# Kernel optimization log

Measured on AMD Instinct MI355X. Metric: run time of the kernel, lower is better.

## Reference

```python
import jax, jax.numpy as jnp
import numpy as np

N, K, IN_DIM, OUT_DIM = 100000, 16, 64, 64
BN_EPS = 1e-5


def setup_inputs() -> dict:
    key = jax.random.key(0)
    ks = jax.random.split(key, 12)
    def lin(k, fan_in, shape):
        bound = 1.0 / np.sqrt(fan_in)
        return jax.random.uniform(k, shape, jnp.float32, -bound, bound)
    return {
        'points': jax.random.normal(ks[0], (N, 3), jnp.float32),
        'neighbors': jax.random.randint(ks[1], (N, K), 0, N + 1, jnp.int32),
        'feats': jax.random.normal(ks[2], (N, IN_DIM), jnp.float32),
        'q_w': lin(ks[3], IN_DIM, (OUT_DIM, IN_DIM)), 'q_b': lin(ks[3], IN_DIM, (OUT_DIM,)),
        'k_w': lin(ks[4], IN_DIM, (OUT_DIM, IN_DIM)), 'k_b': lin(ks[4], IN_DIM, (OUT_DIM,)),
        'v_w': lin(ks[5], IN_DIM, (OUT_DIM, IN_DIM)), 'v_b': lin(ks[5], IN_DIM, (OUT_DIM,)),
        'p_w': lin(ks[6], 3, (OUT_DIM, 3)), 'p_b': lin(ks[6], 3, (OUT_DIM,)),
        'p_gamma': jnp.ones((OUT_DIM,), jnp.float32), 'p_beta': jnp.zeros((OUT_DIM,), jnp.float32),
        'w_w': lin(ks[7], OUT_DIM, (OUT_DIM, OUT_DIM)), 'w_b': lin(ks[7], OUT_DIM, (OUT_DIM,)),
        'w_gamma': jnp.ones((OUT_DIM,), jnp.float32), 'w_beta': jnp.zeros((OUT_DIM,), jnp.float32),
    }


def _bn_relu(x, gamma, beta):
    # BatchNorm1d (training mode, biased var) over all axes except channel (last), then ReLU
    mean = jnp.mean(x, axis=(0, 1), keepdims=True)
    var = jnp.mean(jnp.square(x - mean), axis=(0, 1), keepdims=True)
    y = (x - mean) * jax.lax.rsqrt(var + BN_EPS) * gamma + beta
    return jax.nn.relu(y)


def reference(points, neighbors, feats, q_w, q_b, k_w, k_b, v_w, v_b,
              p_w, p_b, p_gamma, p_beta, w_w, w_b, w_gamma, w_beta):
    q = feats @ q_w.T + q_b                       # [N, D]
    k = feats @ k_w.T + k_b
    v = feats @ v_w.T + v_b
    # shadow-pad with an out-of-range point / zero feats
    points_pad = jnp.concatenate([points, jnp.full((1, 3), 1e6, points.dtype)], 0)
    k_pad = jnp.concatenate([k, jnp.zeros((1, k.shape[1]), k.dtype)], 0)
    v_pad = jnp.concatenate([v, jnp.zeros((1, v.shape[1]), v.dtype)], 0)
    p_g = points_pad[neighbors]                   # [N, K, 3]
    k_g = k_pad[neighbors]                        # [N, K, D]
    v_g = v_pad[neighbors]                        # [N, K, D]
    p_feats = _bn_relu(p_g @ p_w.T + p_b, p_gamma, p_beta)          # [N, K, D]
    w = k_g * q[:, None, :] + p_feats                               # [N, K, D]
    w = _bn_relu(w @ w_w.T + w_b, w_gamma, w_beta)
    w = jax.nn.softmax(w, axis=1)                 # softmax over neighbor axis
    att = jnp.sum((v_g + p_feats) * w, axis=1)    # [N, D]
    return att
```

## Files before the change

### kernel.cpp

```cpp
#include <hip/hip_runtime.h>
#include <math.h>

#define NP 100000
#define KN 16
#define DIM 64
constexpr float BN_EPS_F = 1e-5f;
constexpr double MS = (double)NP * (double)KN;

typedef __attribute__((ext_vector_type(8))) short short8;
typedef __attribute__((ext_vector_type(4))) float f32x4;

constexpr size_t B_S1  = 0;
constexpr size_t B_PWE = 128;
constexpr size_t B_S2  = 1152;
constexpr size_t B_BN2 = 2176;
constexpr size_t B_ZSE = 2688;
constexpr size_t B_ZSB = 2944;
constexpr size_t B_PFS = 3200;
constexpr size_t B_PTS = 4096;
constexpr size_t B_Q   = 1204224;
constexpr size_t B_U   = B_Q + (size_t)NP * DIM * 2;
constexpr size_t B_KK  = B_U + (size_t)(NP + 1) * DIM * 2;
constexpr size_t B_Z1   = B_KK + (size_t)(NP + 1) * DIM * 4;
constexpr size_t B_END1 = B_Z1 + (size_t)NP * 2048;
constexpr size_t B_Z2   = B_KK + (size_t)(NP + 1) * DIM * 2;
constexpr size_t B_END2 = B_Z2 + (size_t)NP * 2048;

__device__ __forceinline__ ushort f2bf(float f) {
  union { float f; unsigned u; } v; v.f = f;
  unsigned u = v.u + 0x7fffu + ((v.u >> 16) & 1u);
  return (ushort)(u >> 16);
}
__device__ __forceinline__ float bf2f(ushort b) {
  union { unsigned u; float f; } v; v.u = ((unsigned)b) << 16;
  return v.f;
}
__device__ __forceinline__ float u2f(unsigned u) {
  union { unsigned u; float f; } v; v.u = u; return v.f;
}

__device__ __forceinline__ void load_wfrags(const float* __restrict__ ww, int lane,
                                            short8 wf[4][2]) {
  int co = lane & 15, g = lane >> 4;
#pragma unroll
  for (int tn = 0; tn < 4; ++tn)
#pragma unroll
    for (int kk = 0; kk < 2; ++kk) {
      const float* p = ww + (size_t)(co + 16 * tn) * DIM + kk * 32 + g * 8;
      short8 f;
#pragma unroll
      for (int j = 0; j < 8; ++j) f[j] = (short)f2bf(p[j]);
      wf[tn][kk] = f;
    }
}

__device__ __forceinline__ short8 pack_bf8(float4 a, float4 b) {
  short8 r;
  r[0] = (short)f2bf(a.x); r[1] = (short)f2bf(a.y);
  r[2] = (short)f2bf(a.z); r[3] = (short)f2bf(a.w);
  r[4] = (short)f2bf(b.x); r[5] = (short)f2bf(b.y);
  r[6] = (short)f2bf(b.z); r[7] = (short)f2bf(b.w);
  return r;
}

__global__ void k_init(char* __restrict__ wsb) {
  int t = threadIdx.x;
  double* s1 = (double*)(wsb + B_S1);
  double* s2 = (double*)(wsb + B_S2);
  if (t < 10) s1[t] = 0.0;
  if (t < 128) s2[t] = 0.0;
  if (t < 32)
    ((unsigned*)(wsb + B_U))[(size_t)NP * 32 + t] = 0u;
}

__global__ __launch_bounds__(256) void k_pts(const float* __restrict__ pts,
                                             char* __restrict__ wsb) {
  int t = blockIdx.x * 256 + threadIdx.x;
  float* p3 = (float*)(wsb + B_PTS);
  if (t < NP * 3) p3[t] = pts[t];
  else if (t < NP * 3 + 3) p3[t] = 1e6f;
}

__global__ __launch_bounds__(256) void k_stats1(const int* __restrict__ nbr,
    char* __restrict__ wsb) {
  const float* p3 = (const float*)(wsb + B_PTS);
  double a[10] = {0, 0, 0, 0, 0, 0, 0, 0, 0, 0};
  int stride = gridDim.x * blockDim.x;
  for (int e = blockIdx.x * 256 + threadIdx.x; e < NP * KN; e += stride) {
    int idx = nbr[e];
    const float* pr = p3 + (size_t)idx * 3;
    float x = pr[0], y = pr[1], z = pr[2];
    a[9] += (idx >= NP) ? 1.0 : 0.0;
    a[0] += x; a[1] += y; a[2] += z;
    a[3] += (double)x * x; a[4] += (double)x * y; a[5] += (double)x * z;
    a[6] += (double)y * y; a[7] += (double)y * z; a[8] += (double)z * z;
  }
  __shared__ double red[256];
  double* s1 = (double*)(wsb + B_S1);
  for (int j = 0; j < 10; ++j) {
    red[threadIdx.x] = a[j];
    __syncthreads();
    for (int s = 128; s > 0; s >>= 1) {
      if (threadIdx.x < s) red[threadIdx.x] += red[threadIdx.x + s];
      __syncthreads();
    }
    if (threadIdx.x == 0) atomicAdd(&s1[j], red[0]);
    __syncthreads();
  }
}

__global__ void k_fold1(const float* __restrict__ pw, const float* __restrict__ pb,
                        const float* __restrict__ pg, const float* __restrict__ pbeta,
                        char* __restrict__ wsb) {
  int c = threadIdx.x;
  if (c >= DIM) return;
  double* s1 = (double*)(wsb + B_S1);
  double inv = 1.0 / MS;
  double m0 = s1[0] * inv, m1 = s1[1] * inv, m2 = s1[2] * inv;
  double C00 = s1[3] * inv - m0 * m0, C01 = s1[4] * inv - m0 * m1;
  double C02 = s1[5] * inv - m0 * m2, C11 = s1[6] * inv - m1 * m1;
  double C12 = s1[7] * inv - m1 * m2, C22 = s1[8] * inv - m2 * m2;
  double w0 = pw[c * 3], w1 = pw[c * 3 + 1], w2 = pw[c * 3 + 2];
  double mean = w0 * m0 + w1 * m1 + w2 * m2 + (double)pb[c];
  double var = w0 * w0 * C00 + w1 * w1 * C11 + w2 * w2 * C22
             + 2.0 * (w0 * w1 * C01 + w0 * w2 * C02 + w1 * w2 * C12);
  if (var < 0.0) var = 0.0;
  double a = (double)pg[c] / sqrt(var + (double)BN_EPS_F);
  float4 o;
  o.x = (float)(w0 * a); o.y = (float)(w1 * a); o.z = (float)(w2 * a);
  o.w = (float)(((double)pb[c] - mean) * a + (double)pbeta[c]);
  ((float4*)(wsb + B_PWE))[c] = o;
}

__global__ void k_shadow(const float* __restrict__ ww, const float* __restrict__ wb,
                         char* __restrict__ wsb, int kpmode) {
  __shared__ float pfs[64], pfb[64];
  int c = threadIdx.x;
  if (c >= DIM) return;
  float4 pwe = ((const float4*)(wsb + B_PWE))[c];
  float pf = fmaxf(fmaf(pwe.x, 1e6f, fmaf(pwe.y, 1e6f, fmaf(pwe.z, 1e6f, pwe.w))), 0.f);
  pfs[c] = pf;
  pfb[c] = bf2f(f2bf(pf));
  ((float*)(wsb + B_PFS))[c] = pf;
  if (kpmode)
    ((unsigned*)(wsb + B_KK))[(size_t)NP * DIM + c] = ((unsigned)f2bf(pf) << 16);
  else
    ((ushort*)(wsb + B_KK))[(size_t)NP * DIM + c] = 0;
  __syncthreads();
  double ze = (double)wb[c], zb = (double)wb[c];
  for (int i = 0; i < DIM; ++i) {
    float w = ww[c * DIM + i];
    ze += (double)pfs[i] * (double)w;
    zb += (double)pfb[i] * (double)bf2f(f2bf(w));
  }
  ((float*)(wsb + B_ZSE))[c] = (float)ze;
  ((float*)(wsb + B_ZSB))[c] = (float)zb;
}

template<bool KPMODE>
__global__ __launch_bounds__(256, 2) void k_qkv_mfma(const float* __restrict__ feats,
    const float* __restrict__ qw, const float* __restrict__ qb,
    const float* __restrict__ kw, const float* __restrict__ kb,
    const float* __restrict__ vw, const float* __restrict__ vb,
    char* __restrict__ wsb) {
  int tid = threadIdx.x, wid = tid >> 6, lane = tid & 63;
  int co = lane & 15, g = lane >> 4;
  short8 wfq[4][2], wfk[4][2], wfv[4][2];
  load_wfrags(qw, lane, wfq);
  load_wfrags(kw, lane, wfk);
  load_wfrags(vw, lane, wfv);
  float bq[4], bk[4], bv[4];
  float4 pwe4[4];
#pragma unroll
  for (int tn = 0; tn < 4; ++tn) {
    bq[tn] = qb[co + 16 * tn];
    bk[tn] = kb[co + 16 * tn];
    bv[tn] = vb[co + 16 * tn];
    pwe4[tn] = ((const float4*)(wsb + B_PWE))[co + 16 * tn];
  }
  const float* p3 = (const float*)(wsb + B_PTS);
  ushort* qt = (ushort*)(wsb + B_Q);
  ushort* ut = (ushort*)(wsb + B_U);
  ushort* kt = (ushort*)(wsb + B_KK);
  unsigned* kpt = (unsigned*)(wsb + B_KK);
  const int NT = NP / 16;
  for (int t = blockIdx.x * 4 + wid; t < NT; t += gridDim.x * 4) {
    const float* fr = feats + ((size_t)t * 16 + co) * DIM + g * 8;
    float4 f0 = *(const float4*)fr;
    float4 f1 = *(const float4*)(fr + 4);
    float4 f2 = *(const float4*)(fr + 32);
    float4 f3 = *(const float4*)(fr + 36);
    short8 a0 = pack_bf8(f0, f1);
    short8 a1 = pack_bf8(f2, f3);
    int nb = t * 16 + g * 4;
    float px[4], py[4], pz[4];
#pragma unroll
    for (int r = 0; r < 4; ++r) {
      const float* pr = p3 + (size_t)(nb + r) * 3;
      px[r] = pr[0]; py[r] = pr[1]; pz[r] = pr[2];
    }
    float pf[4][4];
#pragma unroll
    for (int tn = 0; tn < 4; ++tn)
#pragma unroll
      for (int r = 0; r < 4; ++r)
        pf[tn][r] = fmaxf(fmaf(pwe4[tn].x, px[r], fmaf(pwe4[tn].y, py[r],
                          fmaf(pwe4[tn].z, pz[r], pwe4[tn].w))), 0.f);
#pragma unroll
    for (int tn = 0; tn < 4; ++tn) {
      f32x4 acc = {bq[tn], bq[tn], bq[tn], bq[tn]};
      acc = __builtin_amdgcn_mfma_f32_16x16x32_bf16(a0, wfq[tn][0], acc, 0, 0, 0);
      acc = __builtin_amdgcn_mfma_f32_16x16x32_bf16(a1, wfq[tn][1], acc, 0, 0, 0);
#pragma unroll
      for (int r = 0; r < 4; ++r)
        qt[(size_t)(nb + r) * DIM + co + 16 * tn] = f2bf(acc[r]);
    }
#pragma unroll
    for (int tn = 0; tn < 4; ++tn) {
      f32x4 acc = {bk[tn], bk[tn], bk[tn], bk[tn]};
      acc = __builtin_amdgcn_mfma_f32_16x16x32_bf16(a0, wfk[tn][0], acc, 0, 0, 0);
      acc = __builtin_amdgcn_mfma_f32_16x16x32_bf16(a1, wfk[tn][1], acc, 0, 0, 0);
#pragma unroll
      for (int r = 0; r < 4; ++r) {
        if (KPMODE)
          kpt[(size_t)(nb + r) * DIM + co + 16 * tn] =
              ((unsigned)f2bf(pf[tn][r]) << 16) | (unsigned)f2bf(acc[r]);
        else
          kt[(size_t)(nb + r) * DIM + co + 16 * tn] = f2bf(acc[r]);
      }
    }
#pragma unroll
    for (int tn = 0; tn < 4; ++tn) {
      f32x4 acc = {bv[tn], bv[tn], bv[tn], bv[tn]};
      acc = __builtin_amdgcn_mfma_f32_16x16x32_bf16(a0, wfv[tn][0], acc, 0, 0, 0);
      acc = __builtin_amdgcn_mfma_f32_16x16x32_bf16(a1, wfv[tn][1], acc, 0, 0, 0);
#pragma unroll
      for (int r = 0; r < 4; ++r)
        ut[(size_t)(nb + r) * DIM + co + 16 * tn] = f2bf(acc[r] + pf[tn][r]);
    }
  }
}

#define LOADN(SET, nn) {                                                      \
  const int4* p4_ = (const int4*)(nbr + (size_t)(nn) * KN);                   \
  int4 b0_ = p4_[0], b1_ = p4_[1], b2_ = p4_[2], b3_ = p4_[3];                \
  i##SET[0] = b0_.x; i##SET[1] = b0_.y; i##SET[2] = b0_.z; i##SET[3] = b0_.w; \
  i##SET[4] = b1_.x; i##SET[5] = b1_.y; i##SET[6] = b1_.z; i##SET[7] = b1_.w; \
  i##SET[8] = b2_.x; i##SET[9] = b2_.y; i##SET[10]= b2_.z; i##SET[11]= b2_.w; \
  i##SET[12]= b3_.x; i##SET[13]= b3_.y; i##SET[14]= b3_.z; i##SET[15]= b3_.w; }

#define S2_LOADG(SET, nn) {                                                   \
  if constexpr (KPMODE) {                                                     \
    _Pragma("unroll") for (int k = 0; k < KN; ++k)                            \
      kp##SET[k] = kpt[(size_t)i##SET[k] * DIM + c];                          \
  } else {                                                                    \
    _Pragma("unroll") for (int k = 0; k < KN; ++k) {                          \
      int ik_ = i##SET[k];                                                    \
      unsigned kv_ = kt[(size_t)ik_ * DIM + c];                               \
      const float* pr_ = p3 + (size_t)ik_ * 3;                                \
      float px_ = pr_[0], py_ = pr_[1], pz_ = pr_[2];                         \
      float pf_ = fmaxf(fmaf(pwe.x, px_, fmaf(pwe.y, py_,                     \
                        fmaf(pwe.z, pz_, pwe.w))), 0.f);                      \
      kp##SET[k] = ((unsigned)f2bf(pf_) << 16) | kv_;                         \
    }                                                                         \
  }                                                                           \
  q##SET = bf2f(qt[(size_t)(nn) * DIM + c]); }

#define S2_COMPUTE(SET, nn) {                                                 \
  _Pragma("unroll") for (int k = 0; k < KN; ++k) {                            \
    float kg_ = u2f(kp##SET[k] << 16);                                        \
    float pf_ = u2f(kp##SET[k] & 0xffff0000u);                                \
    hw[k * 64 + (c ^ ((k & 7) << 3))] = f2bf(fmaf(kg_, q##SET, pf_));         \
  }                                                                           \
  __builtin_amdgcn_wave_barrier();                                            \
  short8 a0_ = *(short8*)&hw[aoff0];                                          \
  short8 a1_ = *(short8*)&hw[aoff1];                                          \
  char* zr_ = ztc + (size_t)(nn) * 2048 + g * 8;                              \
  _Pragma("unroll") for (int tn = 0; tn < 4; ++tn) {                          \
    f32x4 acc_ = {wbv[tn], wbv[tn], wbv[tn], wbv[tn]};                        \
    acc_ = __builtin_amdgcn_mfma_f32_16x16x32_bf16(a0_, wf[tn][0], acc_,0,0,0);\
    acc_ = __builtin_amdgcn_mfma_f32_16x16x32_bf16(a1_, wf[tn][1], acc_,0,0,0);\
    _Pragma("unroll") for (int r = 0; r < 4; ++r) {                           \
      float zv_ = acc_[r];                                                    \
      s[tn] += zv_; ssq[tn] = fmaf(zv_, zv_, ssq[tn]); }                      \
    uint2 w_;                                                                 \
    w_.x = (unsigned)f2bf(acc_[0]) | ((unsigned)f2bf(acc_[1]) << 16);         \
    w_.y = (unsigned)f2bf(acc_[2]) | ((unsigned)f2bf(acc_[3]) << 16);         \
    *(uint2*)(zr_ + ((lane & 15) + 16 * tn) * 32) = w_;                       \
  }                                                                           \
  __builtin_amdgcn_wave_barrier(); }

template<bool KPMODE>
__global__ __launch_bounds__(256) void k_stats2(const int* __restrict__ nbr,
    const float* __restrict__ ww, const float* __restrict__ wbias,
    char* __restrict__ wsb, char* __restrict__ ztc) {
  __shared__ ushort hl[4][16 * 64];
  __shared__ float sred[4][64], ssred[4][64];
  int tid = threadIdx.x, wid = tid >> 6, lane = tid & 63, c = lane;
  short8 wf[4][2];
  load_wfrags(ww, lane, wf);
  float wbv[4];
#pragma unroll
  for (int tn = 0; tn < 4; ++tn) wbv[tn] = wbias[(lane & 15) + 16 * tn];
  const ushort* qt = (const ushort*)(wsb + B_Q);
  const ushort* kt = (const ushort*)(wsb + B_KK);
  const unsigned* kpt = (const unsigned*)(wsb + B_KK);
  const float* p3 = (const float*)(wsb + B_PTS);
  float4 pwe = ((const float4*)(wsb + B_PWE))[c];
  ushort* hw = hl[wid];
  int row = lane & 15, g = lane >> 4;
  int aoff0 = row * 64 + ((g * 8) ^ ((row & 7) << 3));
  int aoff1 = row * 64 + ((32 + g * 8) ^ ((row & 7) << 3));
  float s[4] = {0, 0, 0, 0}, ssq[4] = {0, 0, 0, 0};
  const int S = gridDim.x * 4;
  int n = blockIdx.x * 4 + wid;

  int iA[KN], iB[KN];
  unsigned kpA[KN], kpB[KN];
  float qA, qB;

  LOADN(A, n)
  LOADN(B, n + S)
  S2_LOADG(A, n)
  for (int it = 0; it < 4; ++it) {
    S2_LOADG(B, n + S)
    if (it < 3) LOADN(A, n + 2 * S)
    S2_COMPUTE(A, n)
    if (it < 3) { S2_LOADG(A, n + 2 * S) LOADN(B, n + 3 * S) }
    S2_COMPUTE(B, n + S)
    n += 2 * S;
  }
#pragma unroll
  for (int t = 0; t < 4; ++t) {
    s[t] += __shfl_xor(s[t], 16);    s[t] += __shfl_xor(s[t], 32);
    ssq[t] += __shfl_xor(ssq[t], 16); ssq[t] += __shfl_xor(ssq[t], 32);
  }
  if (lane < 16) {
#pragma unroll
    for (int t = 0; t < 4; ++t) { sred[wid][lane + 16 * t] = s[t]; ssred[wid][lane + 16 * t] = ssq[t]; }
  }
  __syncthreads();
  if (tid < DIM) {
    double SS0 = 0.0, SS1 = 0.0;
    for (int w = 0; w < 4; ++w) { SS0 += (double)sred[w][tid]; SS1 += (double)ssred[w][tid]; }
    double* s2 = (double*)(wsb + B_S2);
    atomicAdd(&s2[tid], SS0);
    atomicAdd(&s2[DIM + tid], SS1);
  }
}

__global__ void k_fold2(const float* __restrict__ wg, const float* __restrict__ wbeta,
                        char* __restrict__ wsb) {
  int c = threadIdx.x;
  if (c >= DIM) return;
  double* s2 = (double*)(wsb + B_S2);
  double* s1 = (double*)(wsb + B_S1);
  double nsh = s1[9];
  double zse = (double)((float*)(wsb + B_ZSE))[c];
  double zsb = (double)((float*)(wsb + B_ZSB))[c];
  double S  = s2[c] + nsh * (zse - zsb);
  double SS = s2[DIM + c] + nsh * (zse * zse - zsb * zsb);
  double mean = S / MS;
  double var = SS / MS - mean * mean;
  if (var < 0.0) var = 0.0;
  double a = (double)wg[c] / sqrt(var + (double)BN_EPS_F);
  ((float*)(wsb + B_BN2))[c] = (float)a;
  ((float*)(wsb + B_BN2))[DIM + c] = (float)((double)wbeta[c] - mean * a);
}

#define FS_LOADG(SET, nn) {                                                   \
  const char* zr_ = ztc + (size_t)(nn) * 2048 + c * 32;                       \
  *(uint4*)&zz##SET[0] = *(const uint4*)(zr_);                                \
  *(uint4*)&zz##SET[4] = *(const uint4*)(zr_ + 16);                           \
  _Pragma("unroll") for (int k = 0; k < KN; ++k)                              \
    uv##SET[k] = ut[(size_t)i##SET[k] * DIM + c];                             \
  sh##SET = 0u;                                                               \
  _Pragma("unroll") for (int k = 0; k < KN; ++k)                              \
    sh##SET |= (unsigned)(i##SET[k] >= NP) << k; }

#define FS_COMPUTE(SET, nn) {                                                 \
  float lg_[KN];                                                              \
  float m_ = 0.f;                                                             \
  _Pragma("unroll") for (int k = 0; k < KN; ++k) {                            \
    float lin_ = bf2f((ushort)(zz##SET[k >> 1] >> ((k & 1) * 16)));           \
    if ((sh##SET >> k) & 1u) lin_ = zsec;                                     \
    float t_ = fmaxf(fmaf(lin_, fsc, fsh), 0.f);                              \
    lg_[k] = t_; m_ = fmaxf(m_, t_); }                                        \
  float se_ = 0.f;                                                            \
  _Pragma("unroll") for (int k = 0; k < KN; ++k) {                            \
    float e_ = __expf(lg_[k] - m_); lg_[k] = e_; se_ += e_; }                 \
  float rs_ = 1.0f / se_;                                                     \
  float att_ = 0.f;                                                           \
  _Pragma("unroll") for (int k = 0; k < KN; ++k) {                            \
    float u_ = ((sh##SET >> k) & 1u) ? pfsec : bf2f(uv##SET[k]);              \
    att_ = fmaf(u_, lg_[k] * rs_, att_); }                                    \
  out[(size_t)(nn) * DIM + c] = att_; }

__global__ __launch_bounds__(256) void k_final_str(const int* __restrict__ nbr,
    const char* __restrict__ wsb, const char* __restrict__ ztc,
    float* __restrict__ out) {
  int tid = threadIdx.x, wid = tid >> 6, c = tid & 63;
  const ushort* ut = (const ushort*)(wsb + B_U);
  const float* bn2 = (const float*)(wsb + B_BN2);
  float fsc = bn2[c], fsh = bn2[DIM + c];
  float zsec = ((const float*)(wsb + B_ZSE))[c];
  float pfsec = ((const float*)(wsb + B_PFS))[c];
  const int S = gridDim.x * 4;
  int n = blockIdx.x * 4 + wid;

  int iA[KN], iB[KN];
  unsigned zzA[8], zzB[8];
  ushort uvA[KN], uvB[KN];
  unsigned shA, shB;

  LOADN(A, n)
  LOADN(B, n + S)
  FS_LOADG(A, n)
  for (int it = 0; it < 4; ++it) {
    FS_LOADG(B, n + S)
    if (it < 3) LOADN(A, n + 2 * S)
    FS_COMPUTE(A, n)
    if (it < 3) { FS_LOADG(A, n + 2 * S) LOADN(B, n + 3 * S) }
    FS_COMPUTE(B, n + S)
    n += 2 * S;
  }
}

extern "C" void kernel_launch(void* const* d_in, const int* in_sizes, int n_in,
                              void* d_out, int out_size, void* d_ws, size_t ws_size,
                              hipStream_t stream) {
  const float* pts   = (const float*)d_in[0];
  const int*   nbr   = (const int*)d_in[1];
  const float* feats = (const float*)d_in[2];
  const float* qw = (const float*)d_in[3];  const float* qb = (const float*)d_in[4];
  const float* kw = (const float*)d_in[5];  const float* kb = (const float*)d_in[6];
  const float* vw = (const float*)d_in[7];  const float* vb = (const float*)d_in[8];
  const float* pw = (const float*)d_in[9];  const float* pb = (const float*)d_in[10];
  const float* pg = (const float*)d_in[11]; const float* pbeta = (const float*)d_in[12];
  const float* www = (const float*)d_in[13]; const float* wb = (const float*)d_in[14];
  const float* wg  = (const float*)d_in[15]; const float* wbeta = (const float*)d_in[16];
  char* wsb = (char*)d_ws;
  float* out = (float*)d_out;

  const bool kpmode = (ws_size >= B_END1);
  char* zt = wsb + (kpmode ? B_Z1 : B_Z2);

  hipLaunchKernelGGL(k_init,   dim3(1),    dim3(256), 0, stream, wsb);
  hipLaunchKernelGGL(k_pts,    dim3(1173), dim3(256), 0, stream, pts, wsb);
  hipLaunchKernelGGL(k_stats1, dim3(512),  dim3(256), 0, stream, nbr, wsb);
  hipLaunchKernelGGL(k_fold1,  dim3(1),    dim3(64),  0, stream, pw, pb, pg, pbeta, wsb);
  hipLaunchKernelGGL(k_shadow, dim3(1),    dim3(64),  0, stream, www, wb, wsb, (int)kpmode);
  if (kpmode) {
    hipLaunchKernelGGL((k_qkv_mfma<true>), dim3(256),  dim3(256), 0, stream,
                       feats, qw, qb, kw, kb, vw, vb, wsb);
    hipLaunchKernelGGL((k_stats2<true>),   dim3(3125), dim3(256), 0, stream,
                       nbr, www, wb, wsb, zt);
  } else {
    hipLaunchKernelGGL((k_qkv_mfma<false>), dim3(256),  dim3(256), 0, stream,
                       feats, qw, qb, kw, kb, vw, vb, wsb);
    hipLaunchKernelGGL((k_stats2<false>),   dim3(3125), dim3(256), 0, stream,
                       nbr, www, wb, wsb, zt);
  }
  hipLaunchKernelGGL(k_fold2, dim3(1), dim3(64), 0, stream, wg, wbeta, wsb);
  hipLaunchKernelGGL(k_final_str, dim3(3125), dim3(256), 0, stream, nbr, wsb, zt, out);
}
```

Baseline: 289.6 us.

## Fuse setup kernels, vectorize stats1, and add fragment-layout stats2 kernel

Merges the init and points-copy kernels, and the fold1 and shadow kernels, which removes two tiny launches. Stats1 now reads neighbor indices as int4 with a larger grid. In kpmode, stats2 is replaced by a new kernel where each lane loads contiguous uint4 chunks of one neighbor's packed k/pf row and builds MFMA A fragments directly in registers. This avoids the per-element gathers and the LDS staging of the old path. The new kernel must reproduce the z output layout exactly, and the per-lane vector loads add register pressure.

```diff
diff --git a/kernel.cpp b/kernel.cpp
--- a/kernel.cpp
+++ b/kernel.cpp
@@ -63,37 +63,39 @@
   return r;
 }
 
-__global__ void k_init(char* __restrict__ wsb) {
-  int t = threadIdx.x;
-  double* s1 = (double*)(wsb + B_S1);
-  double* s2 = (double*)(wsb + B_S2);
-  if (t < 10) s1[t] = 0.0;
-  if (t < 128) s2[t] = 0.0;
-  if (t < 32)
-    ((unsigned*)(wsb + B_U))[(size_t)NP * 32 + t] = 0u;
-}
-
-__global__ __launch_bounds__(256) void k_pts(const float* __restrict__ pts,
-                                             char* __restrict__ wsb) {
+__global__ __launch_bounds__(256) void k_init_pts(const float* __restrict__ pts,
+                                                  char* __restrict__ wsb) {
   int t = blockIdx.x * 256 + threadIdx.x;
   float* p3 = (float*)(wsb + B_PTS);
   if (t < NP * 3) p3[t] = pts[t];
   else if (t < NP * 3 + 3) p3[t] = 1e6f;
+  if (blockIdx.x == 0) {
+    int u = threadIdx.x;
+    double* s1 = (double*)(wsb + B_S1);
+    double* s2 = (double*)(wsb + B_S2);
+    if (u < 10) s1[u] = 0.0;
+    if (u < 128) s2[u] = 0.0;
+    if (u < 32) ((unsigned*)(wsb + B_U))[(size_t)NP * 32 + u] = 0u;
+  }
 }
 
 __global__ __launch_bounds__(256) void k_stats1(const int* __restrict__ nbr,
     char* __restrict__ wsb) {
   const float* p3 = (const float*)(wsb + B_PTS);
   double a[10] = {0, 0, 0, 0, 0, 0, 0, 0, 0, 0};
-  int stride = gridDim.x * blockDim.x;
-  for (int e = blockIdx.x * 256 + threadIdx.x; e < NP * KN; e += stride) {
-    int idx = nbr[e];
-    const float* pr = p3 + (size_t)idx * 3;
-    float x = pr[0], y = pr[1], z = pr[2];
-    a[9] += (idx >= NP) ? 1.0 : 0.0;
-    a[0] += x; a[1] += y; a[2] += z;
-    a[3] += (double)x * x; a[4] += (double)x * y; a[5] += (double)x * z;
-    a[6] += (double)y * y; a[7] += (double)y * z; a[8] += (double)z * z;
+  int stride = gridDim.x * 256;
+  for (int e4 = blockIdx.x * 256 + threadIdx.x; e4 < NP * KN / 4; e4 += stride) {
+    int4 b = ((const int4*)nbr)[e4];
+    int id[4] = {b.x, b.y, b.z, b.w};
+#pragma unroll
+    for (int j = 0; j < 4; ++j) {
+      const float* pr = p3 + (size_t)id[j] * 3;
+      float x = pr[0], y = pr[1], z = pr[2];
+      a[9] += (id[j] >= NP) ? 1.0 : 0.0;
+      a[0] += x; a[1] += y; a[2] += z;
+      a[3] += (double)x * x; a[4] += (double)x * y; a[5] += (double)x * z;
+      a[6] += (double)y * y; a[7] += (double)y * z; a[8] += (double)z * z;
+    }
   }
   __shared__ double red[256];
   double* s1 = (double*)(wsb + B_S1);
@@ -109,9 +111,11 @@
   }
 }
 
-__global__ void k_fold1(const float* __restrict__ pw, const float* __restrict__ pb,
-                        const float* __restrict__ pg, const float* __restrict__ pbeta,
-                        char* __restrict__ wsb) {
+__global__ void k_fold1sh(const float* __restrict__ pw, const float* __restrict__ pb,
+                          const float* __restrict__ pg, const float* __restrict__ pbeta,
+                          const float* __restrict__ ww, const float* __restrict__ wb,
+                          char* __restrict__ wsb, int kpmode) {
+  __shared__ float pfs[64], pfb[64];
   int c = threadIdx.x;
   if (c >= DIM) return;
   double* s1 = (double*)(wsb + B_S1);
@@ -130,15 +134,7 @@
   o.x = (float)(w0 * a); o.y = (float)(w1 * a); o.z = (float)(w2 * a);
   o.w = (float)(((double)pb[c] - mean) * a + (double)pbeta[c]);
   ((float4*)(wsb + B_PWE))[c] = o;
-}
-
-__global__ void k_shadow(const float* __restrict__ ww, const float* __restrict__ wb,
-                         char* __restrict__ wsb, int kpmode) {
-  __shared__ float pfs[64], pfb[64];
-  int c = threadIdx.x;
-  if (c >= DIM) return;
-  float4 pwe = ((const float4*)(wsb + B_PWE))[c];
-  float pf = fmaxf(fmaf(pwe.x, 1e6f, fmaf(pwe.y, 1e6f, fmaf(pwe.z, 1e6f, pwe.w))), 0.f);
+  float pf = fmaxf(fmaf(o.x, 1e6f, fmaf(o.y, 1e6f, fmaf(o.z, 1e6f, o.w))), 0.f);
   pfs[c] = pf;
   pfb[c] = bf2f(f2bf(pf));
   ((float*)(wsb + B_PFS))[c] = pf;
@@ -241,6 +237,96 @@
   }
 }
 
+#define SF_LOADN(SET, nn)  i##SET = nbr[(size_t)(nn) * KN + co];
+
+#define SF_LOADG(SET, nn) {                                                   \
+  const uint4* kr_ = (const uint4*)(kpt + (size_t)i##SET * DIM);              \
+  *(uint4*)&kw##SET[0]  = kr_[2 * g];                                         \
+  *(uint4*)&kw##SET[4]  = kr_[2 * g + 1];                                     \
+  *(uint4*)&kw##SET[8]  = kr_[8 + 2 * g];                                     \
+  *(uint4*)&kw##SET[12] = kr_[9 + 2 * g];                                     \
+  const uint4* qr_ = (const uint4*)(qt + (size_t)(nn) * DIM);                 \
+  *(uint4*)&qw##SET[0] = qr_[g];                                              \
+  *(uint4*)&qw##SET[4] = qr_[4 + g]; }
+
+#define SF_COMPUTE(SET, nn) {                                                 \
+  union { unsigned u[4]; short8 s; } a0_, a1_;                                \
+  _Pragma("unroll") for (int p = 0; p < 4; ++p) {                             \
+    unsigned w0_ = kw##SET[2 * p],     w1_ = kw##SET[2 * p + 1];              \
+    unsigned w2_ = kw##SET[8 + 2 * p], w3_ = kw##SET[9 + 2 * p];              \
+    unsigned q0_ = qw##SET[p],         q1_ = qw##SET[4 + p];                  \
+    float h0_ = fmaf(u2f(w0_ << 16), u2f(q0_ << 16),         u2f(w0_ & 0xffff0000u)); \
+    float h1_ = fmaf(u2f(w1_ << 16), u2f(q0_ & 0xffff0000u), u2f(w1_ & 0xffff0000u)); \
+    float h2_ = fmaf(u2f(w2_ << 16), u2f(q1_ << 16),         u2f(w2_ & 0xffff0000u)); \
+    float h3_ = fmaf(u2f(w3_ << 16), u2f(q1_ & 0xffff0000u), u2f(w3_ & 0xffff0000u)); \
+    a0_.u[p] = (unsigned)f2bf(h0_) | ((unsigned)f2bf(h1_) << 16);             \
+    a1_.u[p] = (unsigned)f2bf(h2_) | ((unsigned)f2bf(h3_) << 16);             \
+  }                                                                           \
+  char* zr_ = ztc + (size_t)(nn) * 2048 + g * 8;                              \
+  _Pragma("unroll") for (int tn = 0; tn < 4; ++tn) {                          \
+    f32x4 acc_ = {wbv[tn], wbv[tn], wbv[tn], wbv[tn]};                        \
+    acc_ = __builtin_amdgcn_mfma_f32_16x16x32_bf16(a0_.s, wf[tn][0], acc_,0,0,0); \
+    acc_ = __builtin_amdgcn_mfma_f32_16x16x32_bf16(a1_.s, wf[tn][1], acc_,0,0,0); \
+    _Pragma("unroll") for (int r = 0; r < 4; ++r) {                           \
+      float zv_ = acc_[r];                                                    \
+      s[tn] += zv_; ssq[tn] = fmaf(zv_, zv_, ssq[tn]); }                      \
+    uint2 wz_;                                                                \
+    wz_.x = (unsigned)f2bf(acc_[0]) | ((unsigned)f2bf(acc_[1]) << 16);        \
+    wz_.y = (unsigned)f2bf(acc_[2]) | ((unsigned)f2bf(acc_[3]) << 16);        \
+    *(uint2*)(zr_ + (co + 16 * tn) * 32) = wz_;                               \
+  } }
+
+__global__ __launch_bounds__(256) void k_stats2_frag(const int* __restrict__ nbr,
+    const float* __restrict__ ww, const float* __restrict__ wbias,
+    char* __restrict__ wsb, char* __restrict__ ztc) {
+  __shared__ float sred[4][64], ssred[4][64];
+  int tid = threadIdx.x, wid = tid >> 6, lane = tid & 63;
+  int co = lane & 15, g = lane >> 4;
+  short8 wf[4][2];
+  load_wfrags(ww, lane, wf);
+  float wbv[4];
+#pragma unroll
+  for (int tn = 0; tn < 4; ++tn) wbv[tn] = wbias[co + 16 * tn];
+  const ushort* qt = (const ushort*)(wsb + B_Q);
+  const unsigned* kpt = (const unsigned*)(wsb + B_KK);
+  float s[4] = {0, 0, 0, 0}, ssq[4] = {0, 0, 0, 0};
+  const int S = gridDim.x * 4;
+  int n = blockIdx.x * 4 + wid;
+
+  int iA, iB;
+  unsigned kwA[16], kwB[16], qwA[8], qwB[8];
+
+  SF_LOADN(A, n)
+  SF_LOADN(B, n + S)
+  SF_LOADG(A, n)
+#pragma unroll 1
+  for (int it = 0; it < 4; ++it) {
+    SF_LOADG(B, n + S)
+    if (it < 3) SF_LOADN(A, n + 2 * S)
+    SF_COMPUTE(A, n)
+    if (it < 3) { SF_LOADG(A, n + 2 * S) SF_LOADN(B, n + 3 * S) }
+    SF_COMPUTE(B, n + S)
+    n += 2 * S;
+  }
+#pragma unroll
+  for (int t = 0; t < 4; ++t) {
+    s[t] += __shfl_xor(s[t], 16);    s[t] += __shfl_xor(s[t], 32);
+    ssq[t] += __shfl_xor(ssq[t], 16); ssq[t] += __shfl_xor(ssq[t], 32);
+  }
+  if (lane < 16) {
+#pragma unroll
+    for (int t = 0; t < 4; ++t) { sred[wid][lane + 16 * t] = s[t]; ssred[wid][lane + 16 * t] = ssq[t]; }
+  }
+  __syncthreads();
+  if (tid < DIM) {
+    double SS0 = 0.0, SS1 = 0.0;
+    for (int w = 0; w < 4; ++w) { SS0 += (double)sred[w][tid]; SS1 += (double)ssred[w][tid]; }
+    double* s2 = (double*)(wsb + B_S2);
+    atomicAdd(&s2[tid], SS0);
+    atomicAdd(&s2[DIM + tid], SS1);
+  }
+}
+
 #define LOADN(SET, nn) {                                                      \
   const int4* p4_ = (const int4*)(nbr + (size_t)(nn) * KN);                   \
   int4 b0_ = p4_[0], b1_ = p4_[1], b2_ = p4_[2], b3_ = p4_[3];                \
@@ -249,24 +335,19 @@
   i##SET[8] = b2_.x; i##SET[9] = b2_.y; i##SET[10]= b2_.z; i##SET[11]= b2_.w; \
   i##SET[12]= b3_.x; i##SET[13]= b3_.y; i##SET[14]= b3_.z; i##SET[15]= b3_.w; }
 
-#define S2_LOADG(SET, nn) {                                                   \
-  if constexpr (KPMODE) {                                                     \
-    _Pragma("unroll") for (int k = 0; k < KN; ++k)                            \
-      kp##SET[k] = kpt[(size_t)i##SET[k] * DIM + c];                          \
-  } else {                                                                    \
-    _Pragma("unroll") for (int k = 0; k < KN; ++k) {                          \
-      int ik_ = i##SET[k];                                                    \
-      unsigned kv_ = kt[(size_t)ik_ * DIM + c];                               \
-      const float* pr_ = p3 + (size_t)ik_ * 3;                                \
-      float px_ = pr_[0], py_ = pr_[1], pz_ = pr_[2];                         \
-      float pf_ = fmaxf(fmaf(pwe.x, px_, fmaf(pwe.y, py_,                     \
-                        fmaf(pwe.z, pz_, pwe.w))), 0.f);                      \
-      kp##SET[k] = ((unsigned)f2bf(pf_) << 16) | kv_;                         \
-    }                                                                         \
+#define S2T_LOADG(SET, nn) {                                                  \
+  _Pragma("unroll") for (int k = 0; k < KN; ++k) {                            \
+    int ik_ = i##SET[k];                                                      \
+    unsigned kv_ = kt[(size_t)ik_ * DIM + c];                                 \
+    const float* pr_ = p3 + (size_t)ik_ * 3;                                  \
+    float px_ = pr_[0], py_ = pr_[1], pz_ = pr_[2];                           \
+    float pf_ = fmaxf(fmaf(pwe.x, px_, fmaf(pwe.y, py_,                       \
+                      fmaf(pwe.z, pz_, pwe.w))), 0.f);                        \
+    kp##SET[k] = ((unsigned)f2bf(pf_) << 16) | kv_;                           \
   }                                                                           \
   q##SET = bf2f(qt[(size_t)(nn) * DIM + c]); }
 
-#define S2_COMPUTE(SET, nn) {                                                 \
+#define S2T_COMPUTE(SET, nn) {                                                \
   _Pragma("unroll") for (int k = 0; k < KN; ++k) {                            \
     float kg_ = u2f(kp##SET[k] << 16);                                        \
     float pf_ = u2f(kp##SET[k] & 0xffff0000u);                                \
@@ -290,8 +371,7 @@
   }                                                                           \
   __builtin_amdgcn_wave_barrier(); }
 
-template<bool KPMODE>
-__global__ __launch_bounds__(256) void k_stats2(const int* __restrict__ nbr,
+__global__ __launch_bounds__(256) void k_stats2_t2(const int* __restrict__ nbr,
     const float* __restrict__ ww, const float* __restrict__ wbias,
     char* __restrict__ wsb, char* __restrict__ ztc) {
   __shared__ ushort hl[4][16 * 64];
@@ -304,7 +384,6 @@
   for (int tn = 0; tn < 4; ++tn) wbv[tn] = wbias[(lane & 15) + 16 * tn];
   const ushort* qt = (const ushort*)(wsb + B_Q);
   const ushort* kt = (const ushort*)(wsb + B_KK);
-  const unsigned* kpt = (const unsigned*)(wsb + B_KK);
   const float* p3 = (const float*)(wsb + B_PTS);
   float4 pwe = ((const float4*)(wsb + B_PWE))[c];
   ushort* hw = hl[wid];
@@ -321,13 +400,13 @@
 
   LOADN(A, n)
   LOADN(B, n + S)
-  S2_LOADG(A, n)
+  S2T_LOADG(A, n)
   for (int it = 0; it < 4; ++it) {
-    S2_LOADG(B, n + S)
+    S2T_LOADG(B, n + S)
     if (it < 3) LOADN(A, n + 2 * S)
-    S2_COMPUTE(A, n)
-    if (it < 3) { S2_LOADG(A, n + 2 * S) LOADN(B, n + 3 * S) }
-    S2_COMPUTE(B, n + S)
+    S2T_COMPUTE(A, n)
+    if (it < 3) { S2T_LOADG(A, n + 2 * S) LOADN(B, n + 3 * S) }
+    S2T_COMPUTE(B, n + S)
     n += 2 * S;
   }
 #pragma unroll
@@ -445,20 +524,19 @@
   const bool kpmode = (ws_size >= B_END1);
   char* zt = wsb + (kpmode ? B_Z1 : B_Z2);
 
-  hipLaunchKernelGGL(k_init,   dim3(1),    dim3(256), 0, stream, wsb);
-  hipLaunchKernelGGL(k_pts,    dim3(1173), dim3(256), 0, stream, pts, wsb);
-  hipLaunchKernelGGL(k_stats1, dim3(512),  dim3(256), 0, stream, nbr, wsb);
-  hipLaunchKernelGGL(k_fold1,  dim3(1),    dim3(64),  0, stream, pw, pb, pg, pbeta, wsb);
-  hipLaunchKernelGGL(k_shadow, dim3(1),    dim3(64),  0, stream, www, wb, wsb, (int)kpmode);
+  hipLaunchKernelGGL(k_init_pts, dim3(1173), dim3(256), 0, stream, pts, wsb);
+  hipLaunchKernelGGL(k_stats1,   dim3(1024), dim3(256), 0, stream, nbr, wsb);
+  hipLaunchKernelGGL(k_fold1sh,  dim3(1),    dim3(64),  0, stream,
+                     pw, pb, pg, pbeta, www, wb, wsb, (int)kpmode);
   if (kpmode) {
     hipLaunchKernelGGL((k_qkv_mfma<true>), dim3(256),  dim3(256), 0, stream,
                        feats, qw, qb, kw, kb, vw, vb, wsb);
-    hipLaunchKernelGGL((k_stats2<true>),   dim3(3125), dim3(256), 0, stream,
+    hipLaunchKernelGGL(k_stats2_frag,      dim3(3125), dim3(256), 0, stream,
                        nbr, www, wb, wsb, zt);
   } else {
     hipLaunchKernelGGL((k_qkv_mfma<false>), dim3(256),  dim3(256), 0, stream,
                        feats, qw, qb, kw, kb, vw, vb, wsb);
-    hipLaunchKernelGGL((k_stats2<false>),   dim3(3125), dim3(256), 0, stream,
+    hipLaunchKernelGGL(k_stats2_t2,         dim3(3125), dim3(256), 0, stream,
                        nbr, www, wb, wsb, zt);
   }
   hipLaunchKernelGGL(k_fold2, dim3(1), dim3(64), 0, stream, wg, wbeta, wsb);
```

After: 341.2 us. 17.8% more time.
